# Kernel optimization log

Measured on AMD Instinct MI355X. Metric: run time of the kernel, lower is better.

The kernel has to match this reference:

```python
import jax, jax.numpy as jnp
import numpy as np

DIM_MODEL = 512
DIM_HEAD = 64


def setup_inputs() -> dict:
    key = jax.random.key(0)
    ks = jax.random.split(key, 7)
    B, S = 4, 4096
    scale = 1.0 / np.sqrt(DIM_MODEL)
    x = jax.random.normal(ks[0], (B, S, DIM_MODEL), dtype=jnp.float32)
    # nn.Linear weights: stored as [out, in] in torch; we use [in, out] for x @ W
    Wq = jax.random.uniform(ks[1], (DIM_MODEL, DIM_HEAD), jnp.float32, -scale, scale)
    Wk = jax.random.uniform(ks[2], (DIM_MODEL, DIM_HEAD), jnp.float32, -scale, scale)
    Wv = jax.random.uniform(ks[3], (DIM_MODEL, DIM_HEAD), jnp.float32, -scale, scale)
    bq = jax.random.uniform(ks[4], (DIM_HEAD,), jnp.float32, -scale, scale)
    bk = jax.random.uniform(ks[5], (DIM_HEAD,), jnp.float32, -scale, scale)
    bv = jax.random.uniform(ks[6], (DIM_HEAD,), jnp.float32, -scale, scale)
    return {"x": x, "Wq": Wq, "bq": bq, "Wk": Wk, "bk": bk, "Wv": Wv, "bv": bv}


def reference(x, Wq, bq, Wk, bk, Wv, bv):
    # [q,k,v] = z @ U_qkv
    q = x @ Wq + bq  # [B, S, Dh]
    k = x @ Wk + bk
    v = x @ Wv + bv
    dot_scale = jnp.sqrt(jnp.asarray(DIM_HEAD, dtype=x.dtype))
    scores = jnp.einsum("bsd,btd->bst", q, k) / dot_scale  # [B, S, S]
    attn = jax.nn.softmax(scores, axis=-1)
    return jnp.einsum("bst,btd->bsd", attn, v)  # [B, S, Dh]
```

## Files before the change

### kernel.cpp

```cpp
#include <hip/hip_runtime.h>
#include <hip/hip_bf16.h>

typedef short short8 __attribute__((ext_vector_type(8)));
typedef float f32x4 __attribute__((ext_vector_type(4)));

#define MFMA16(a,b,c) __builtin_amdgcn_mfma_f32_16x16x32_bf16((a),(b),(c),0,0,0)

#define NROWS 16384
#define LOG2E 1.44269504088896340736f

#define OFF_Q  0u
#define OFF_K  (2u<<20)
#define OFF_V  (4u<<20)
#define OFF_W  (6u<<20)
#define OFF_O  ((6u<<20) + (1u<<18))

__device__ __forceinline__ unsigned short f2bf(float f){
    union { float f; unsigned u; } v; v.f = f;
    unsigned r = v.u + 0x7FFFu + ((v.u >> 16) & 1u);
    return (unsigned short)(r >> 16);
}
__device__ __forceinline__ unsigned pk2(float a, float b){
    union { __hip_bfloat162 h; unsigned u; } c;
    c.h = __float22bfloat162_rn(make_float2(a, b));
    return c.u;
}

union Frag {
    short8 s;
    unsigned short u[8];
    uint2 d2[2];
    uint4 q4;
};

__global__ __launch_bounds__(256) void wprep_kernel(
    const float* __restrict__ Wq, const float* __restrict__ Wk,
    const float* __restrict__ Wv, unsigned short* __restrict__ wfrag)
{
    int idx = blockIdx.x * 256 + threadIdx.x;
    int lane = idx & 63;
    int rest = idx >> 6;
    int kk = rest & 15;
    int nt = (rest >> 4) & 3;
    int w  = rest >> 6;
    const float* W = (w == 0) ? Wq : (w == 1) ? Wk : Wv;
    float scl = (w == 0) ? (0.125f * LOG2E) : 1.0f;
    int n = 16 * nt + (lane & 15);
    int g = lane >> 4;
    Frag o;
#pragma unroll
    for (int e = 0; e < 8; ++e) {
        int k = 32 * kk + 16 * (e >> 2) + 4 * g + (e & 3);
        o.u[e] = f2bf(W[k * 64 + n] * scl);
    }
    *(uint4*)(wfrag + (size_t)idx * 8) = o.q4;
}

__global__ __launch_bounds__(192) void qkv_kernel(
    const float* __restrict__ x,
    const float* __restrict__ bq, const float* __restrict__ bk,
    const float* __restrict__ bv,
    const unsigned short* __restrict__ wfrag,
    unsigned short* __restrict__ qfrag,
    unsigned short* __restrict__ kfrag,
    unsigned short* __restrict__ vfrag)
{
    __shared__ unsigned short xs[16][520];
    const int tid = threadIdx.x;
    const int lane = tid & 63;
    const int w = tid >> 6;
    const int l15 = lane & 15, g = lane >> 4;
    const int rg = blockIdx.x;
    const float* xbase = x + (size_t)rg * 16 * 512;

    for (int i = tid; i < 2048; i += 192) {
        float4 v = *(const float4*)(xbase + i * 4);
        int r_ = i >> 7;
        int c_ = (i & 127) * 4;
        *(uint2*)&xs[r_][c_] = make_uint2(pk2(v.x, v.y), pk2(v.z, v.w));
    }
    __syncthreads();

    f32x4 acc[4];
#pragma unroll
    for (int nt = 0; nt < 4; ++nt) acc[nt] = (f32x4){0.f,0.f,0.f,0.f};

    const uint4* wf = (const uint4*)wfrag + (size_t)w * 4096;

#pragma unroll
    for (int kk = 0; kk < 16; ++kk) {
        Frag xf;
        xf.d2[0] = *(const uint2*)&xs[l15][32 * kk + 4 * g];
        xf.d2[1] = *(const uint2*)&xs[l15][32 * kk + 16 + 4 * g];

        Frag wr[4];
#pragma unroll
        for (int nt = 0; nt < 4; ++nt)
            wr[nt].q4 = wf[((size_t)nt * 16 + kk) * 64 + lane];

        if (w == 2) {
#pragma unroll
            for (int nt = 0; nt < 4; ++nt) acc[nt] = MFMA16(xf.s, wr[nt].s, acc[nt]);
        } else {
#pragma unroll
            for (int nt = 0; nt < 4; ++nt) acc[nt] = MFMA16(wr[nt].s, xf.s, acc[nt]);
        }
    }

    const int b   = rg >> 8;
    const int rgb = rg & 255;
    const int tc  = rgb >> 2;
    const int c   = rgb & 3;

    if (w == 0) {
#pragma unroll
        for (int nt = 0; nt < 4; ++nt) {
            float4 bb = *(const float4*)(bq + 16 * nt + 4 * g);
            const float bs = 0.125f * LOG2E;
            float q0 = acc[nt][0] + bb.x * bs;
            float q1 = acc[nt][1] + bb.y * bs;
            float q2 = acc[nt][2] + bb.z * bs;
            float q3 = acc[nt][3] + bb.w * bs;
            int ks = nt >> 1, h = nt & 1;
            size_t qoff = ((size_t)(rg * 2 + ks) * 64 + lane) * 8 + h * 4;
            *(uint2*)(qfrag + qoff) = make_uint2(pk2(q0, q1), pk2(q2, q3));
        }
    } else if (w == 1) {
#pragma unroll
        for (int nt = 0; nt < 4; ++nt) {
            float4 bb = *(const float4*)(bk + 16 * nt + 4 * g);
            float k0 = acc[nt][0] + bb.x;
            float k1 = acc[nt][1] + bb.y;
            float k2 = acc[nt][2] + bb.z;
            float k3 = acc[nt][3] + bb.w;
            int ks = nt >> 1, h = nt & 1;
            size_t kfi = ((size_t)((b * 64 + tc) * 4 + c) * 2 + ks);
            size_t koff = (kfi * 64 + lane) * 8 + h * 4;
            *(uint2*)(kfrag + koff) = make_uint2(pk2(k0, k1), pk2(k2, k3));
        }
    } else {
        const int vks = c >> 1, vh = c & 1;
#pragma unroll
        for (int nt = 0; nt < 4; ++nt) {
            float bvv = bv[16 * nt + l15];
            float v0 = acc[nt][0] + bvv;
            float v1 = acc[nt][1] + bvv;
            float v2 = acc[nt][2] + bvv;
            float v3 = acc[nt][3] + bvv;
            size_t vfi = ((size_t)((b * 64 + tc) * 4 + nt) * 2 + vks);
            size_t voff = (vfi * 64 + lane) * 8 + vh * 4;
            *(uint2*)(vfrag + voff) = make_uint2(pk2(v0, v1), pk2(v2, v3));
        }
    }
}

#define LOADK(KD, CH) do { \
    const size_t b_ = ((size_t)(tcg0 + (CH)) * 8) * 64 + lane; \
    _Pragma("unroll") \
    for (int c_ = 0; c_ < 4; ++c_) { \
        KD[c_][0].q4 = kf4[b_ + (size_t)(c_ * 2 + 0) * 64]; \
        KD[c_][1].q4 = kf4[b_ + (size_t)(c_ * 2 + 1) * 64]; \
    } } while (0)

#define BODY(KC, KN, CH, CHN) do { \
    Frag vC[4][2]; \
    { const size_t b_ = ((size_t)(tcg0 + (CH)) * 8) * 64 + lane; \
      _Pragma("unroll") \
      for (int c_ = 0; c_ < 4; ++c_) { \
        vC[c_][0].q4 = vf4[b_ + (size_t)(c_ * 2 + 0) * 64]; \
        vC[c_][1].q4 = vf4[b_ + (size_t)(c_ * 2 + 1) * 64]; \
      } } \
    _Pragma("unroll") \
    for (int M_ = 0; M_ < 2; ++M_) { \
        f32x4 sD[4]; \
        _Pragma("unroll") \
        for (int c_ = 0; c_ < 4; ++c_) { \
            f32x4 D = (f32x4){0.f,0.f,0.f,0.f}; \
            D = MFMA16(KC[c_][0].s, qf[M_][0].s, D); \
            D = MFMA16(KC[c_][1].s, qf[M_][1].s, D); \
            sD[c_] = D; \
        } \
        if (M_ == 0) LOADK(KN, CHN); \
        Frag pa0, pa1; \
        float lloc = 0.f; \
        _Pragma("unroll") \
        for (int c_ = 0; c_ < 4; ++c_) { \
            float p0 = __builtin_exp2f(sD[c_][0]); \
            float p1 = __builtin_exp2f(sD[c_][1]); \
            float p2 = __builtin_exp2f(sD[c_][2]); \
            float p3 = __builtin_exp2f(sD[c_][3]); \
            lloc += (p0 + p1) + (p2 + p3); \
            uint2 pk_ = make_uint2(pk2(p0, p1), pk2(p2, p3)); \
            if (c_ < 2) pa0.d2[c_ & 1] = pk_; else pa1.d2[c_ & 1] = pk_; \
        } \
        l_run[M_] += lloc; \
        _Pragma("unroll") \
        for (int dc_ = 0; dc_ < 4; ++dc_) { \
            acc[M_][dc_] = MFMA16(pa0.s, vC[dc_][0].s, acc[M_][dc_]); \
            acc[M_][dc_] = MFMA16(pa1.s, vC[dc_][1].s, acc[M_][dc_]); \
        } \
    } } while (0)

__global__ __launch_bounds__(256, 3) void attn_kernel(
    const unsigned short* __restrict__ qfrag,
    const unsigned short* __restrict__ kfrag,
    const unsigned short* __restrict__ vfrag,
    uint2* __restrict__ OpartU, float* __restrict__ lml, int CPS)
{
    const int tid = threadIdx.x;
    const int lane = tid & 63;
    const int w = tid >> 6;
    const int l15 = lane & 15, g = lane >> 4;
    const int qblock = blockIdx.x & 127;
    const int split  = blockIdx.x >> 7;
    const int gw = qblock * 4 + w;
    const int b = gw >> 7;
    const int tcg0 = b * 64 + split * CPS;

    const uint4* qf4 = (const uint4*)qfrag;
    const uint4* kf4 = (const uint4*)kfrag;
    const uint4* vf4 = (const uint4*)vfrag;

    Frag qf[2][2];
#pragma unroll
    for (int M = 0; M < 2; ++M)
#pragma unroll
        for (int ks = 0; ks < 2; ++ks)
            qf[M][ks].q4 = qf4[((size_t)((gw * 2 + M) * 2 + ks)) * 64 + lane];

    f32x4 acc[2][4];
#pragma unroll
    for (int M = 0; M < 2; ++M)
#pragma unroll
        for (int dc = 0; dc < 4; ++dc) acc[M][dc] = (f32x4){0.f,0.f,0.f,0.f};
    float l_run[2] = {0.f, 0.f};

    Frag kA[4][2], kB[4][2];
    LOADK(kA, 0);

#pragma unroll 1
    for (int ch = 0; ch < CPS; ch += 2) {
        int n2 = (ch + 2 < CPS) ? (ch + 2) : ch;
        BODY(kA, kB, ch, ch + 1);
        BODY(kB, kA, ch + 1, n2);
    }

#pragma unroll
    for (int M = 0; M < 2; ++M) {
        float lt = l_run[M];
        lt += __shfl_xor(lt, 16);
        lt += __shfl_xor(lt, 32);
#pragma unroll
        for (int dc = 0; dc < 4; ++dc)
            OpartU[((size_t)(split * 512 + gw) * 8 + M * 4 + dc) * 64 + lane] =
                make_uint2(pk2(acc[M][dc][0], acc[M][dc][1]),
                           pk2(acc[M][dc][2], acc[M][dc][3]));
        if (g == 0)
            lml[(size_t)(split * 512 + gw) * 32 + M * 16 + l15] = lt;
    }
}

__global__ __launch_bounds__(256) void merge_kernel(
    const uint2* __restrict__ OpartU, const float* __restrict__ lml,
    float* __restrict__ out, int S)
{
    int gid = blockIdx.x * 256 + threadIdx.x;
    int lane = gid & 63;
    int dc = (gid >> 6) & 3;
    int M  = (gid >> 8) & 1;
    int gw = gid >> 9;
    int l15 = lane & 15, g = lane >> 4;

    float o0 = 0.f, o1 = 0.f, o2 = 0.f, o3 = 0.f;
    float L0 = 0.f, L1 = 0.f, L2 = 0.f, L3 = 0.f;
    for (int s = 0; s < S; ++s) {
        uint2 pv = OpartU[((size_t)(s * 512 + gw) * 8 + M * 4 + dc) * 64 + lane];
        float4 lv = *(const float4*)(lml + (size_t)(s * 512 + gw) * 32 + M * 16 + 4 * g);
        o0 += __uint_as_float(pv.x << 16);
        o1 += __uint_as_float(pv.x & 0xFFFF0000u);
        o2 += __uint_as_float(pv.y << 16);
        o3 += __uint_as_float(pv.y & 0xFFFF0000u);
        L0 += lv.x; L1 += lv.y; L2 += lv.z; L3 += lv.w;
    }
    size_t row = (size_t)gw * 32 + M * 16 + 4 * g;
    int col = 16 * dc + l15;
    out[(row + 0) * 64 + col] = o0 / L0;
    out[(row + 1) * 64 + col] = o1 / L1;
    out[(row + 2) * 64 + col] = o2 / L2;
    out[(row + 3) * 64 + col] = o3 / L3;
}

extern "C" void kernel_launch(void* const* d_in, const int* in_sizes, int n_in,
                              void* d_out, int out_size, void* d_ws, size_t ws_size,
                              hipStream_t stream) {
    (void)in_sizes; (void)n_in; (void)out_size;
    const float* x  = (const float*)d_in[0];
    const float* Wq = (const float*)d_in[1];
    const float* bq = (const float*)d_in[2];
    const float* Wk = (const float*)d_in[3];
    const float* bk = (const float*)d_in[4];
    const float* Wv = (const float*)d_in[5];
    const float* bv = (const float*)d_in[6];
    float* out = (float*)d_out;

    char* ws = (char*)d_ws;
    unsigned short* qfrag = (unsigned short*)(ws + OFF_Q);
    unsigned short* kfrag = (unsigned short*)(ws + OFF_K);
    unsigned short* vfrag = (unsigned short*)(ws + OFF_V);
    unsigned short* wfrag = (unsigned short*)(ws + OFF_W);

    const size_t oneO = (size_t)512 * 8 * 64 * 8;
    const size_t oneL = (size_t)512 * 32 * 4;
    int S = 8;
    if (ws_size < (size_t)OFF_O + 8 * (oneO + oneL)) S = 4;
    if (ws_size < (size_t)OFF_O + 4 * (oneO + oneL)) S = 2;
    uint2* OpartU = (uint2*)(ws + OFF_O);
    float* lml    = (float*)(ws + OFF_O + (size_t)S * oneO);
    int CPS = 64 / S;

    hipLaunchKernelGGL(wprep_kernel, dim3(48), dim3(256), 0, stream,
                       Wq, Wk, Wv, wfrag);
    hipLaunchKernelGGL(qkv_kernel, dim3(1024), dim3(192), 0, stream,
                       x, bq, bk, bv, wfrag, qfrag, kfrag, vfrag);
    hipLaunchKernelGGL(attn_kernel, dim3(128 * S), dim3(256), 0, stream,
                       qfrag, kfrag, vfrag, OpartU, lml, CPS);
    hipLaunchKernelGGL(merge_kernel, dim3(1024), dim3(256), 0, stream,
                       OpartU, lml, out, S);
}
```

Baseline: 70.12 us.

## Double-buffer V fragments with K and interleave split blocks in grid order

V fragments now get the same register double-buffering as K, so the K and V loads for the next chunk are issued at the top of each body, ahead of the current chunk's MFMAs. This removes the exposed V load latency at the start of each chunk. The launch-bounds occupancy hint drops from 3 to 2 waves per SIMD to make room for the extra registers. The block index mapping now puts the split in the low bits, so blocks for the same query block but different key splits run next to each other.

```diff
diff --git a/kernel.cpp b/kernel.cpp
--- a/kernel.cpp
+++ b/kernel.cpp
@@ -154,22 +154,18 @@
     }
 }
 
-#define LOADK(KD, CH) do { \
+#define LOADKV(KD, VD, CH) do { \
     const size_t b_ = ((size_t)(tcg0 + (CH)) * 8) * 64 + lane; \
     _Pragma("unroll") \
     for (int c_ = 0; c_ < 4; ++c_) { \
         KD[c_][0].q4 = kf4[b_ + (size_t)(c_ * 2 + 0) * 64]; \
         KD[c_][1].q4 = kf4[b_ + (size_t)(c_ * 2 + 1) * 64]; \
+        VD[c_][0].q4 = vf4[b_ + (size_t)(c_ * 2 + 0) * 64]; \
+        VD[c_][1].q4 = vf4[b_ + (size_t)(c_ * 2 + 1) * 64]; \
     } } while (0)
 
-#define BODY(KC, KN, CH, CHN) do { \
-    Frag vC[4][2]; \
-    { const size_t b_ = ((size_t)(tcg0 + (CH)) * 8) * 64 + lane; \
-      _Pragma("unroll") \
-      for (int c_ = 0; c_ < 4; ++c_) { \
-        vC[c_][0].q4 = vf4[b_ + (size_t)(c_ * 2 + 0) * 64]; \
-        vC[c_][1].q4 = vf4[b_ + (size_t)(c_ * 2 + 1) * 64]; \
-      } } \
+#define BODY(KC, VC, KN, VN, CHN) do { \
+    LOADKV(KN, VN, CHN); \
     _Pragma("unroll") \
     for (int M_ = 0; M_ < 2; ++M_) { \
         f32x4 sD[4]; \
@@ -180,7 +176,6 @@
             D = MFMA16(KC[c_][1].s, qf[M_][1].s, D); \
             sD[c_] = D; \
         } \
-        if (M_ == 0) LOADK(KN, CHN); \
         Frag pa0, pa1; \
         float lloc = 0.f; \
         _Pragma("unroll") \
@@ -196,23 +191,24 @@
         l_run[M_] += lloc; \
         _Pragma("unroll") \
         for (int dc_ = 0; dc_ < 4; ++dc_) { \
-            acc[M_][dc_] = MFMA16(pa0.s, vC[dc_][0].s, acc[M_][dc_]); \
-            acc[M_][dc_] = MFMA16(pa1.s, vC[dc_][1].s, acc[M_][dc_]); \
+            acc[M_][dc_] = MFMA16(pa0.s, VC[dc_][0].s, acc[M_][dc_]); \
+            acc[M_][dc_] = MFMA16(pa1.s, VC[dc_][1].s, acc[M_][dc_]); \
         } \
     } } while (0)
 
-__global__ __launch_bounds__(256, 3) void attn_kernel(
+__global__ __launch_bounds__(256, 2) void attn_kernel(
     const unsigned short* __restrict__ qfrag,
     const unsigned short* __restrict__ kfrag,
     const unsigned short* __restrict__ vfrag,
-    uint2* __restrict__ OpartU, float* __restrict__ lml, int CPS)
+    uint2* __restrict__ OpartU, float* __restrict__ lml,
+    int CPS, int SBITS)
 {
     const int tid = threadIdx.x;
     const int lane = tid & 63;
     const int w = tid >> 6;
     const int l15 = lane & 15, g = lane >> 4;
-    const int qblock = blockIdx.x & 127;
-    const int split  = blockIdx.x >> 7;
+    const int split  = blockIdx.x & ((1 << SBITS) - 1);
+    const int qblock = blockIdx.x >> SBITS;
     const int gw = qblock * 4 + w;
     const int b = gw >> 7;
     const int tcg0 = b * 64 + split * CPS;
@@ -235,14 +231,15 @@
         for (int dc = 0; dc < 4; ++dc) acc[M][dc] = (f32x4){0.f,0.f,0.f,0.f};
     float l_run[2] = {0.f, 0.f};
 
-    Frag kA[4][2], kB[4][2];
-    LOADK(kA, 0);
+    Frag kA[4][2], kB[4][2], vA[4][2], vB[4][2];
+    LOADKV(kA, vA, 0);
 
 #pragma unroll 1
     for (int ch = 0; ch < CPS; ch += 2) {
-        int n2 = (ch + 2 < CPS) ? (ch + 2) : ch;
-        BODY(kA, kB, ch, ch + 1);
-        BODY(kB, kA, ch + 1, n2);
+        int c1 = (ch + 1 < CPS) ? (ch + 1) : ch;
+        int c2 = (ch + 2 < CPS) ? (ch + 2) : ch;
+        BODY(kA, vA, kB, vB, c1);
+        BODY(kB, vB, kA, vA, c2);
     }
 
 #pragma unroll
@@ -311,9 +308,9 @@
 
     const size_t oneO = (size_t)512 * 8 * 64 * 8;
     const size_t oneL = (size_t)512 * 32 * 4;
-    int S = 8;
-    if (ws_size < (size_t)OFF_O + 8 * (oneO + oneL)) S = 4;
-    if (ws_size < (size_t)OFF_O + 4 * (oneO + oneL)) S = 2;
+    int S = 8, SBITS = 3;
+    if (ws_size < (size_t)OFF_O + 8 * (oneO + oneL)) { S = 4; SBITS = 2; }
+    if (ws_size < (size_t)OFF_O + 4 * (oneO + oneL)) { S = 2; SBITS = 1; }
     uint2* OpartU = (uint2*)(ws + OFF_O);
     float* lml    = (float*)(ws + OFF_O + (size_t)S * oneO);
     int CPS = 64 / S;
@@ -323,7 +320,7 @@
     hipLaunchKernelGGL(qkv_kernel, dim3(1024), dim3(192), 0, stream,
                        x, bq, bk, bv, wfrag, qfrag, kfrag, vfrag);
     hipLaunchKernelGGL(attn_kernel, dim3(128 * S), dim3(256), 0, stream,
-                       qfrag, kfrag, vfrag, OpartU, lml, CPS);
+                       qfrag, kfrag, vfrag, OpartU, lml, CPS, SBITS);
     hipLaunchKernelGGL(merge_kernel, dim3(1024), dim3(256), 0, stream,
                        OpartU, lml, out, S);
 }
```

Result: no change. 69.25 us (-1.2%).
